# Kernel tuning notes

Hardware: AMD Instinct MI355X
Metric: run time of the kernel (lower is better)

The kernel has to match this reference:

```python
import jax, jax.numpy as jnp
import numpy as np

HIDDEN, MSG, KEY, ROUNDS = 256, 64, 16, 2
LN_EPS = 1e-5


def _orthogonal(key, shape, gain):
    # mimic torch orthogonal_ init (exact values don't matter for correctness testing)
    a = jax.random.normal(key, shape, dtype=jnp.float32)
    q, r = jnp.linalg.qr(a.T if shape[0] < shape[1] else a)
    q = q * jnp.sign(jnp.diag(r))
    if shape[0] < shape[1]:
        q = q.T
    return gain * q[:shape[0], :shape[1]]


def setup_inputs() -> dict:
    key = jax.random.key(0)
    ks = jax.random.split(key, 6)
    g = float(np.sqrt(2.0))
    N = 8192
    return {
        "hidden_states": jax.random.normal(ks[0], (N, HIDDEN), dtype=jnp.float32),
        "W_msg": _orthogonal(ks[1], (MSG, HIDDEN), g),
        "b_msg": jnp.zeros((MSG,), jnp.float32),
        "W_key": _orthogonal(ks[2], (KEY, HIDDEN), g),
        "b_key": jnp.zeros((KEY,), jnp.float32),
        "W_qry": _orthogonal(ks[3], (KEY, HIDDEN), g),
        "b_qry": jnp.zeros((KEY,), jnp.float32),
        "W_agg": _orthogonal(ks[4], (HIDDEN, HIDDEN + MSG), g),
        "b_agg": jnp.zeros((HIDDEN,), jnp.float32),
        "ln_g": jnp.ones((HIDDEN,), jnp.float32),
        "ln_b": jnp.zeros((HIDDEN,), jnp.float32),
    }


def reference(hidden_states, W_msg, b_msg, W_key, b_key, W_qry, b_qry,
              W_agg, b_agg, ln_g, ln_b):
    inv_sqrt_k = 1.0 / np.sqrt(KEY)
    h = hidden_states
    attn = None
    for _ in range(ROUNDS):
        msgs = h @ W_msg.T + b_msg          # (N, MSG)
        keys = h @ W_key.T + b_key          # (N, KEY)
        qrys = h @ W_qry.T + b_qry          # (N, KEY)
        scores = (qrys @ keys.T) * inv_sqrt_k  # (N, N)
        attn = jax.nn.softmax(scores, axis=-1)
        agg_msg = attn @ msgs               # (N, MSG)
        combined = jnp.concatenate([h, agg_msg], axis=-1)  # (N, HIDDEN+MSG)
        z = combined @ W_agg.T + b_agg      # (N, HIDDEN)
        mu = jnp.mean(z, axis=-1, keepdims=True)
        var = jnp.mean(jnp.square(z - mu), axis=-1, keepdims=True)
        h = jax.nn.relu(ln_g * (z - mu) * jax.lax.rsqrt(var + LN_EPS) + ln_b)
    return h, attn
```

## Files before the change

### kernel.cpp

```cpp
#include <hip/hip_runtime.h>

constexpr int H = 256, MSGC = 64;
constexpr float LN_EPS = 1e-5f;
constexpr float QSCALE = 0.25f * 1.4426950408889634f;

typedef __attribute__((ext_vector_type(8))) short bf16x8;
typedef __attribute__((ext_vector_type(4))) float f32x4;

__device__ inline ushort f2bf(float x) {
    union { float f; unsigned u; } v; v.f = x;
    unsigned r = v.u + 0x7fffu + ((v.u >> 16) & 1u);
    return (ushort)(r >> 16);
}
__device__ inline float bf2f(ushort h) {
    union { unsigned u; float f; } v; v.u = ((unsigned)h) << 16;
    return v.f;
}
__device__ inline bf16x8 pack_bf16x8(float4 f0, float4 f1) {
    union { unsigned u[4]; bf16x8 v; } cv;
    asm("v_cvt_pk_bf16_f32 %0, %1, %2" : "=v"(cv.u[0]) : "v"(f0.x), "v"(f0.y));
    asm("v_cvt_pk_bf16_f32 %0, %1, %2" : "=v"(cv.u[1]) : "v"(f0.z), "v"(f0.w));
    asm("v_cvt_pk_bf16_f32 %0, %1, %2" : "=v"(cv.u[2]) : "v"(f1.x), "v"(f1.y));
    asm("v_cvt_pk_bf16_f32 %0, %1, %2" : "=v"(cv.u[3]) : "v"(f1.z), "v"(f1.w));
    return cv.v;
}

__global__ __launch_bounds__(256) void prep_kernel(
    const float* __restrict__ Wm, const float* __restrict__ Wk,
    const float* __restrict__ Wq, const float* __restrict__ Wa,
    ushort* __restrict__ Wph, ushort* __restrict__ Wpl,
    ushort* __restrict__ Wfh, ushort* __restrict__ Wfl)
{
    const int t = threadIdx.x, b = blockIdx.x;
    if (b < 48) {
        const int tile = b >> 3, kc = b & 7;
#pragma unroll
        for (int j2 = 0; j2 < 2; ++j2) {
            const int idx = t * 2 + j2;
            const int l = idx >> 3, e = idx & 7;
            const int col = tile * 16 + (l & 15);
            const int k = kc * 32 + (l >> 4) * 8 + e;
            float v;
            if (col < 64)      v = Wm[(size_t)col * H + k];
            else if (col < 80) v = Wk[(size_t)(col - 64) * H + k];
            else               v = QSCALE * Wq[(size_t)(col - 80) * H + k];
            ushort hi = f2bf(v);
            Wph[(size_t)b * 512 + idx] = hi;
            Wpl[(size_t)b * 512 + idx] = f2bf(v - bf2f(hi));
        }
    } else {
        const int unit = b - 48;
        const int ctg = unit / 10, kc = unit % 10;
#pragma unroll
        for (int j2 = 0; j2 < 2; ++j2) {
            const int idx = t * 2 + j2;
            const int l = idx >> 3, e = idx & 7;
            const int col = ctg * 16 + (l & 15);
            const int k = kc * 32 + (l >> 4) * 8 + e;
            const float v = Wa[(size_t)col * 320 + k];
            ushort hi = f2bf(v);
            Wfh[(size_t)unit * 512 + idx] = hi;
            Wfl[(size_t)unit * 512 + idx] = f2bf(v - bf2f(hi));
        }
    }
}

__global__ __launch_bounds__(128) void proj_kernel(
    const float* __restrict__ h,
    const ushort* __restrict__ Wph, const ushort* __restrict__ Wpl,
    const float* __restrict__ bm, const float* __restrict__ bk, const float* __restrict__ bq,
    ushort* __restrict__ msgsF, ushort* __restrict__ kh, ushort* __restrict__ kl,
    ushort* __restrict__ qh, ushort* __restrict__ ql, int n)
{
    constexpr int AST = 264;
    __shared__ ushort Ahi[16 * AST];
    __shared__ ushort Alo[16 * AST];
    const int t = threadIdx.x, lane = t & 63, w = t >> 6;
    const int gq = lane >> 4, c = lane & 15;
    const int r0 = blockIdx.x * 16;
    const float4* hsrc = (const float4*)(h + (size_t)r0 * H);
#pragma unroll
    for (int u = 0; u < 8; ++u) {
        const int idx = t + 128 * u;
        const int row = idx >> 6, c4 = idx & 63;
        float4 v = hsrc[idx];
        ushort4 hi, lo;
        hi.x = f2bf(v.x); lo.x = f2bf(v.x - bf2f(hi.x));
        hi.y = f2bf(v.y); lo.y = f2bf(v.y - bf2f(hi.y));
        hi.z = f2bf(v.z); lo.z = f2bf(v.z - bf2f(hi.z));
        hi.w = f2bf(v.w); lo.w = f2bf(v.w - bf2f(hi.w));
        *(ushort4*)&Ahi[row * AST + c4 * 4] = hi;
        *(ushort4*)&Alo[row * AST + c4 * 4] = lo;
    }
    __syncthreads();
    f32x4 acc[3] = {{0,0,0,0},{0,0,0,0},{0,0,0,0}};
    for (int kc = 0; kc < 8; ++kc) {
        const bf16x8 afh = *(const bf16x8*)&Ahi[c * AST + kc * 32 + gq * 8];
        const bf16x8 afl = *(const bf16x8*)&Alo[c * AST + kc * 32 + gq * 8];
#pragma unroll
        for (int ct = 0; ct < 3; ++ct) {
            const int unit = (w * 3 + ct) * 8 + kc;
            const bf16x8 whi = *(const bf16x8*)(Wph + (size_t)unit * 512 + lane * 8);
            const bf16x8 wlo = *(const bf16x8*)(Wpl + (size_t)unit * 512 + lane * 8);
            acc[ct] = __builtin_amdgcn_mfma_f32_16x16x32_bf16(afh, whi, acc[ct], 0, 0, 0);
            acc[ct] = __builtin_amdgcn_mfma_f32_16x16x32_bf16(afh, wlo, acc[ct], 0, 0, 0);
            acc[ct] = __builtin_amdgcn_mfma_f32_16x16x32_bf16(afl, whi, acc[ct], 0, 0, 0);
        }
    }
#pragma unroll
    for (int ct = 0; ct < 3; ++ct) {
        const int tile = w * 3 + ct;
        if (tile < 4) {
            const float bb = bm[tile * 16 + c];
#pragma unroll
            for (int r = 0; r < 4; ++r) {
                const int j = r0 + gq * 4 + r;
                const size_t idx = ((size_t)(j >> 5) * 4 + tile) * 512
                                 + ((j >> 3) & 3) * 128 + c * 8 + (j & 7);
                msgsF[idx] = f2bf(acc[ct][r] + bb);
            }
        } else if (tile == 4) {
            const float bb = bk[c];
#pragma unroll
            for (int r = 0; r < 4; ++r) {
                const int j = r0 + gq * 4 + r;
                const float v = acc[ct][r] + bb;
                const ushort hi = f2bf(v);
                kh[(size_t)j * 16 + c] = hi;
                kl[(size_t)j * 16 + c] = f2bf(v - bf2f(hi));
            }
        } else {
            const float bb = QSCALE * bq[c];
#pragma unroll
            for (int r = 0; r < 4; ++r) {
                const int j = r0 + gq * 4 + r;
                const float v = acc[ct][r] + bb;
                const ushort hi = f2bf(v);
                qh[(size_t)j * 16 + c] = hi;
                ql[(size_t)j * 16 + c] = f2bf(v - bf2f(hi));
            }
        }
    }
}

__device__ __forceinline__ void loadK(bf16x8* dst, const ushort* __restrict__ kh,
                                      int j0, int g, int c) {
#pragma unroll
    for (int js = 0; js < 4; ++js)
        dst[js] = *(const bf16x8*)(kh + (size_t)(j0 + js * 16 + c) * 16 + 8 * (g & 1));
}

__device__ __forceinline__ void qk_tile(const bf16x8* b1s, const ushort* __restrict__ kl,
                                        int j0, int g, int c, bf16x8 a1, bf16x8 a2,
                                        const bf16x8 zer, f32x4* pd) {
    const f32x4 z4 = {0.f, 0.f, 0.f, 0.f};
    bf16x8 b2s[4];
#pragma unroll
    for (int js = 0; js < 4; ++js)
        b2s[js] = (g < 2) ? *(const bf16x8*)(kl + (size_t)(j0 + js * 16 + c) * 16 + 8 * g) : zer;
#pragma unroll
    for (int js = 0; js < 4; ++js) {
        pd[js] = __builtin_amdgcn_mfma_f32_16x16x32_bf16(a1, b1s[js], z4, 0, 0, 0);
        pd[js] = __builtin_amdgcn_mfma_f32_16x16x32_bf16(a2, b2s[js], pd[js], 0, 0, 0);
    }
}

__device__ __forceinline__ void pv_tile(const float* __restrict__ P,
                                        const ushort* __restrict__ msgsF,
                                        int j0, int g, int c, int w, int lane, f32x4* accv) {
#pragma unroll
    for (int ks = 0; ks < 2; ++ks) {
        const int arow = w * 16 + c;
        const int sw = (arow & 7) << 2;
        const int colb = ks * 32 + 8 * g;
        float4 f0 = *(const float4*)&P[arow * 64 + ((colb) ^ sw)];
        float4 f1 = *(const float4*)&P[arow * 64 + ((colb + 4) ^ sw)];
        bf16x8 af = pack_bf16x8(f0, f1);
        const size_t mbase = ((size_t)(j0 >> 5) + ks) * 4;
#pragma unroll
        for (int mt = 0; mt < 4; ++mt) {
            bf16x8 bfr = *((const bf16x8*)(msgsF + (mbase + mt) * 512) + lane);
            accv[mt] = __builtin_amdgcn_mfma_f32_16x16x32_bf16(af, bfr, accv[mt], 0, 0, 0);
        }
    }
}

__global__ __launch_bounds__(256) void flash1_kernel(
    const ushort* __restrict__ qh, const ushort* __restrict__ ql,
    const ushort* __restrict__ kh, const ushort* __restrict__ kl,
    const ushort* __restrict__ msgsF,
    float* __restrict__ aggO, float* __restrict__ aggL, int n)
{
    __shared__ float P[64 * 64];
    const int t = threadIdx.x, lane = t & 63, w = t >> 6;
    const int g = lane >> 4, c = lane & 15;
    const int i0 = blockIdx.x * 64;
    bf16x8 zer = {0,0,0,0,0,0,0,0};
    f32x4 z4 = {0.f, 0.f, 0.f, 0.f};
    const ushort* qsrc = (g < 2) ? qh : ql;
    bf16x8 a1 = *(const bf16x8*)(qsrc + (size_t)(i0 + w * 16 + c) * 16 + 8 * (g & 1));
    bf16x8 a2 = (g < 2) ? a1 : zer;
    float l[4] = {0.f, 0.f, 0.f, 0.f};
    f32x4 accv[4] = {z4, z4, z4, z4};
    const int nj = n / 8, jb = blockIdx.y * nj;
    bf16x8 bA[4], bB[4];
    loadK(bA, kh, jb, g, c);
    for (int p = 0; p < 8; ++p) {
        const int t0 = jb + p * 128, t1 = t0 + 64;
        const int t2 = (p < 7) ? t0 + 128 : t1;
        loadK(bB, kh, t1, g, c);
        {
            f32x4 pd[4];
            qk_tile(bA, kl, t0, g, c, a1, a2, zer, pd);
#pragma unroll
            for (int js = 0; js < 4; ++js)
#pragma unroll
                for (int r = 0; r < 4; ++r) {
                    const int row = w * 16 + g * 4 + r;
                    float pp = exp2f(pd[js][r]);
                    l[r] += pp;
                    P[row * 64 + ((js * 16 + c) ^ ((row & 7) << 2))] = pp;
                }
            pv_tile(P, msgsF, t0, g, c, w, lane, accv);
        }
        loadK(bA, kh, t2, g, c);
        {
            f32x4 pd[4];
            qk_tile(bB, kl, t1, g, c, a1, a2, zer, pd);
#pragma unroll
            for (int js = 0; js < 4; ++js)
#pragma unroll
                for (int r = 0; r < 4; ++r) {
                    const int row = w * 16 + g * 4 + r;
                    float pp = exp2f(pd[js][r]);
                    l[r] += pp;
                    P[row * 64 + ((js * 16 + c) ^ ((row & 7) << 2))] = pp;
                }
            pv_tile(P, msgsF, t1, g, c, w, lane, accv);
        }
    }
#pragma unroll
    for (int r = 0; r < 4; ++r)
#pragma unroll
        for (int d2 = 1; d2 < 16; d2 <<= 1) l[r] += __shfl_xor(l[r], d2, 64);
#pragma unroll
    for (int mt = 0; mt < 4; ++mt)
#pragma unroll
        for (int r = 0; r < 4; ++r)
            aggO[((size_t)blockIdx.y * n + i0 + w * 16 + g * 4 + r) * MSGC + mt * 16 + c] = accv[mt][r];
    if (c == 0) {
#pragma unroll
        for (int r = 0; r < 4; ++r)
            aggL[(size_t)blockIdx.y * n + i0 + w * 16 + g * 4 + r] = l[r];
    }
}

__global__ __launch_bounds__(256) void stats_kernel(
    const ushort* __restrict__ qh, const ushort* __restrict__ ql,
    const ushort* __restrict__ kh, const ushort* __restrict__ kl,
    float* __restrict__ rowl_p, int n)
{
    const int t = threadIdx.x, lane = t & 63, w = t >> 6;
    const int g = lane >> 4, c = lane & 15;
    const int iq = blockIdx.x * 64 + w * 16 + c;
    bf16x8 zer = {0,0,0,0,0,0,0,0};
    const ushort* qsrc = (g < 2) ? qh : ql;
    bf16x8 a1 = *(const bf16x8*)(qsrc + (size_t)iq * 16 + 8 * (g & 1));
    bf16x8 a2 = (g < 2) ? a1 : zer;
    const int nj = n / 8, jb = blockIdx.y * nj;
    float l[4] = {0.f, 0.f, 0.f, 0.f};
    bf16x8 bA[4], bB[4];
    loadK(bA, kh, jb, g, c);
    for (int p = 0; p < 8; ++p) {
        const int t0 = jb + p * 128, t1 = t0 + 64;
        const int t2 = (p < 7) ? t0 + 128 : t1;
        loadK(bB, kh, t1, g, c);
        {
            f32x4 pd[4];
            qk_tile(bA, kl, t0, g, c, a1, a2, zer, pd);
#pragma unroll
            for (int js = 0; js < 4; ++js)
#pragma unroll
                for (int r = 0; r < 4; ++r) l[r] += exp2f(pd[js][r]);
        }
        loadK(bA, kh, t2, g, c);
        {
            f32x4 pd[4];
            qk_tile(bB, kl, t1, g, c, a1, a2, zer, pd);
#pragma unroll
            for (int js = 0; js < 4; ++js)
#pragma unroll
                for (int r = 0; r < 4; ++r) l[r] += exp2f(pd[js][r]);
        }
    }
#pragma unroll
    for (int r = 0; r < 4; ++r)
#pragma unroll
        for (int d2 = 1; d2 < 16; d2 <<= 1) l[r] += __shfl_xor(l[r], d2, 64);
    if (c == 0) {
        const int q0 = blockIdx.x * 64 + w * 16 + g * 4;
#pragma unroll
        for (int r = 0; r < 4; ++r)
            rowl_p[(size_t)blockIdx.y * n + q0 + r] = l[r];
    }
}

__global__ __launch_bounds__(256) void pass2_kernel(
    const ushort* __restrict__ qh, const ushort* __restrict__ ql,
    const ushort* __restrict__ kh, const ushort* __restrict__ kl,
    const ushort* __restrict__ msgsF, const float* __restrict__ rowl_p,
    float* __restrict__ aggO, float* __restrict__ attn, int n)
{
    __shared__ float P[64 * 64];
    const int t = threadIdx.x, lane = t & 63, w = t >> 6;
    const int g = lane >> 4, c = lane & 15;
    const int i0 = blockIdx.x * 64;
    bf16x8 zer = {0,0,0,0,0,0,0,0};
    f32x4 z4 = {0.f, 0.f, 0.f, 0.f};
    const ushort* qsrc = (g < 2) ? qh : ql;
    bf16x8 a1 = *(const bf16x8*)(qsrc + (size_t)(i0 + w * 16 + c) * 16 + 8 * (g & 1));
    bf16x8 a2 = (g < 2) ? a1 : zer;
    float rinv_r[4];
#pragma unroll
    for (int r = 0; r < 4; ++r) {
        const int q = i0 + w * 16 + g * 4 + r;
        float L = 0.f;
#pragma unroll
        for (int p = 0; p < 8; ++p) L += rowl_p[(size_t)p * n + q];
        rinv_r[r] = 1.f / L;
    }
    f32x4 accv[4] = {z4, z4, z4, z4};
    const int nj = n / 8, jb = blockIdx.y * nj;
    bf16x8 bA[4], bB[4];
    loadK(bA, kh, jb, g, c);
    for (int p = 0; p < 8; ++p) {
        const int t0 = jb + p * 128, t1 = t0 + 64;
        const int t2 = (p < 7) ? t0 + 128 : t1;
        loadK(bB, kh, t1, g, c);
#pragma unroll
        for (int half = 0; half < 2; ++half) {
            const int j0 = half ? t1 : t0;
            f32x4 pd[4];
            qk_tile(half ? bB : bA, kl, j0, g, c, a1, a2, zer, pd);
            if (half == 0) loadK(bA, kh, t2, g, c);
#pragma unroll
            for (int js = 0; js < 4; ++js)
#pragma unroll
                for (int r = 0; r < 4; ++r) {
                    const int row = w * 16 + g * 4 + r;
                    const float pp = exp2f(pd[js][r]) * rinv_r[r];
                    P[row * 64 + ((js * 16 + c) ^ ((row & 7) << 2))] = pp;
                }
#pragma unroll
            for (int u = 0; u < 16; ++u) {
                const int row = w * 16 + u;
                const int sw = (row & 7) << 2;
                attn[(size_t)(i0 + row) * n + j0 + lane] = P[row * 64 + (lane ^ sw)];
            }
            pv_tile(P, msgsF, j0, g, c, w, lane, accv);
        }
    }
#pragma unroll
    for (int mt = 0; mt < 4; ++mt)
#pragma unroll
        for (int r = 0; r < 4; ++r) {
            const int row = w * 16 + g * 4 + r;
            aggO[((size_t)blockIdx.y * n + i0 + row) * MSGC + mt * 16 + c] = accv[mt][r];
        }
}

template <bool FLASH>
__global__ __launch_bounds__(256) void aggln_kernel(
    const float* __restrict__ h, const float* __restrict__ aggO,
    const float* __restrict__ aggL,
    const ushort* __restrict__ Wfh, const ushort* __restrict__ Wfl,
    const float* __restrict__ ba,
    const float* __restrict__ gg, const float* __restrict__ bb,
    float* __restrict__ hout, int n)
{
    constexpr int AST = 328;
    __shared__ ushort Ahi[16 * AST];
    __shared__ ushort Alo[16 * AST];
    __shared__ float Linv[16];
    __shared__ float red1[16][4], red2[16][4];
    const int t = threadIdx.x, lane = t & 63, w = t >> 6;
    const int gq = lane >> 4, c = lane & 15;
    const int r0 = blockIdx.x * 16;
    const float4* hsrc = (const float4*)(h + (size_t)r0 * H);
#pragma unroll
    for (int u = 0; u < 4; ++u) {
        const int idx = t + 256 * u;
        const int row = idx >> 6, c4 = idx & 63;
        float4 v = hsrc[idx];
        ushort4 hi, lo;
        hi.x = f2bf(v.x); lo.x = f2bf(v.x - bf2f(hi.x));
        hi.y = f2bf(v.y); lo.y = f2bf(v.y - bf2f(hi.y));
        hi.z = f2bf(v.z); lo.z = f2bf(v.z - bf2f(hi.z));
        hi.w = f2bf(v.w); lo.w = f2bf(v.w - bf2f(hi.w));
        *(ushort4*)&Ahi[row * AST + c4 * 4] = hi;
        *(ushort4*)&Alo[row * AST + c4 * 4] = lo;
    }
    if (FLASH && t < 16) {
        float L = 0.f;
#pragma unroll
        for (int p = 0; p < 8; ++p) L += aggL[(size_t)p * n + r0 + t];
        Linv[t] = 1.f / L;
    }
    __syncthreads();
    {
        const int row = t >> 4, c4 = t & 15;
        float4 s = {0.f, 0.f, 0.f, 0.f};
#pragma unroll
        for (int p = 0; p < 8; ++p) {
            const float4 v = *(const float4*)(aggO + (size_t)p * n * MSGC
                               + (size_t)(r0 + row) * MSGC + c4 * 4);
            s.x += v.x; s.y += v.y; s.z += v.z; s.w += v.w;
        }
        if (FLASH) { const float li = Linv[row]; s.x *= li; s.y *= li; s.z *= li; s.w *= li; }
        ushort4 hi, lo;
        hi.x = f2bf(s.x); lo.x = f2bf(s.x - bf2f(hi.x));
        hi.y = f2bf(s.y); lo.y = f2bf(s.y - bf2f(hi.y));
        hi.z = f2bf(s.z); lo.z = f2bf(s.z - bf2f(hi.z));
        hi.w = f2bf(s.w); lo.w = f2bf(s.w - bf2f(hi.w));
        *(ushort4*)&Ahi[row * AST + 256 + c4 * 4] = hi;
        *(ushort4*)&Alo[row * AST + 256 + c4 * 4] = lo;
    }
    __syncthreads();
    f32x4 acc[4] = {{0,0,0,0},{0,0,0,0},{0,0,0,0},{0,0,0,0}};
    for (int kc = 0; kc < 10; ++kc) {
        const bf16x8 afh = *(const bf16x8*)&Ahi[c * AST + kc * 32 + gq * 8];
        const bf16x8 afl = *(const bf16x8*)&Alo[c * AST + kc * 32 + gq * 8];
#pragma unroll
        for (int ct = 0; ct < 4; ++ct) {
            const int ctg = w * 4 + ct;
            const bf16x8 whi = *(const bf16x8*)(Wfh + ((size_t)(ctg * 10 + kc)) * 512 + lane * 8);
            const bf16x8 wlo = *(const bf16x8*)(Wfl + ((size_t)(ctg * 10 + kc)) * 512 + lane * 8);
            acc[ct] = __builtin_amdgcn_mfma_f32_16x16x32_bf16(afh, whi, acc[ct], 0, 0, 0);
            acc[ct] = __builtin_amdgcn_mfma_f32_16x16x32_bf16(afh, wlo, acc[ct], 0, 0, 0);
            acc[ct] = __builtin_amdgcn_mfma_f32_16x16x32_bf16(afl, whi, acc[ct], 0, 0, 0);
        }
    }
    float bav[4], gv[4], bv[4];
#pragma unroll
    for (int ct = 0; ct < 4; ++ct) {
        const int col = w * 64 + ct * 16 + c;
        bav[ct] = ba[col]; gv[ct] = gg[col]; bv[ct] = bb[col];
    }
#pragma unroll
    for (int ct = 0; ct < 4; ++ct) {
        acc[ct][0] += bav[ct]; acc[ct][1] += bav[ct];
        acc[ct][2] += bav[ct]; acc[ct][3] += bav[ct];
    }
#pragma unroll
    for (int r = 0; r < 4; ++r) {
        float s1 = 0.f, s2 = 0.f;
#pragma unroll
        for (int ct = 0; ct < 4; ++ct) { const float v = acc[ct][r]; s1 += v; s2 += v * v; }
#pragma unroll
        for (int d = 1; d < 16; d <<= 1) { s1 += __shfl_xor(s1, d, 64); s2 += __shfl_xor(s2, d, 64); }
        if (c == 0) { red1[gq * 4 + r][w] = s1; red2[gq * 4 + r][w] = s2; }
    }
    __syncthreads();
#pragma unroll
    for (int r = 0; r < 4; ++r) {
        const int row = gq * 4 + r;
        const float s1 = red1[row][0] + red1[row][1] + red1[row][2] + red1[row][3];
        const float s2 = red2[row][0] + red2[row][1] + red2[row][2] + red2[row][3];
        const float mu = s1 * (1.f / 256.f);
        const float var = s2 * (1.f / 256.f) - mu * mu;
        const float rs = rsqrtf(var + LN_EPS);
#pragma unroll
        for (int ct = 0; ct < 4; ++ct) {
            float o = (acc[ct][r] - mu) * rs * gv[ct] + bv[ct];
            hout[(size_t)(r0 + row) * H + w * 64 + ct * 16 + c] = fmaxf(o, 0.f);
        }
    }
}

extern "C" void kernel_launch(void* const* d_in, const int* in_sizes, int n_in,
                              void* d_out, int out_size, void* d_ws, size_t ws_size,
                              hipStream_t stream)
{
    const float* hs = (const float*)d_in[0];
    const float* Wm = (const float*)d_in[1];
    const float* bm = (const float*)d_in[2];
    const float* Wk = (const float*)d_in[3];
    const float* bk = (const float*)d_in[4];
    const float* Wq = (const float*)d_in[5];
    const float* bq = (const float*)d_in[6];
    const float* Wa = (const float*)d_in[7];
    const float* ba = (const float*)d_in[8];
    const float* lg = (const float*)d_in[9];
    const float* lb = (const float*)d_in[10];
    const int n = in_sizes[0] / H;

    char* wp = (char*)d_ws;
    auto alloc = [&](size_t bytes) { void* p = (void*)wp; wp += (bytes + 255) & ~(size_t)255; return p; };
    float*  h2     = (float*)alloc((size_t)n * H * 4);
    ushort* qh     = (ushort*)alloc((size_t)n * 16 * 2);
    ushort* ql     = (ushort*)alloc((size_t)n * 16 * 2);
    ushort* kh     = (ushort*)alloc((size_t)n * 16 * 2);
    ushort* kl     = (ushort*)alloc((size_t)n * 16 * 2);
    ushort* msgsF  = (ushort*)alloc((size_t)MSGC * n * 2);
    float*  rowl_p = (float*)alloc((size_t)8 * n * 4);
    float*  aggO   = (float*)alloc((size_t)8 * n * MSGC * 4);
    float*  aggL   = (float*)alloc((size_t)8 * n * 4);
    ushort* Wph    = (ushort*)alloc((size_t)48 * 512 * 2);
    ushort* Wpl    = (ushort*)alloc((size_t)48 * 512 * 2);
    ushort* Wfh    = (ushort*)alloc((size_t)160 * 512 * 2);
    ushort* Wfl    = (ushort*)alloc((size_t)160 * 512 * 2);

    float* hOut = (float*)d_out;
    float* attn = hOut + (size_t)n * H;

    prep_kernel<<<208, 256, 0, stream>>>(Wm, Wk, Wq, Wa, Wph, Wpl, Wfh, Wfl);

    proj_kernel<<<n / 16, 128, 0, stream>>>(hs, Wph, Wpl, bm, bk, bq, msgsF, kh, kl, qh, ql, n);
    flash1_kernel<<<dim3(n / 64, 8), 256, 0, stream>>>(qh, ql, kh, kl, msgsF,
                                                       aggO, aggL, n);
    aggln_kernel<true><<<n / 16, 256, 0, stream>>>(hs, aggO, aggL, Wfh, Wfl,
                                                   ba, lg, lb, h2, n);
    proj_kernel<<<n / 16, 128, 0, stream>>>(h2, Wph, Wpl, bm, bk, bq, msgsF, kh, kl, qh, ql, n);
    stats_kernel<<<dim3(n / 64, 8), 256, 0, stream>>>(qh, ql, kh, kl, rowl_p, n);
    pass2_kernel<<<dim3(n / 64, 8), 256, 0, stream>>>(qh, ql, kh, kl, msgsF,
                                                      rowl_p, aggO, attn, n);
    aggln_kernel<false><<<n / 16, 256, 0, stream>>>(h2, aggO, aggL, Wfh, Wfl,
                                                    ba, lg, lb, hOut, n);
}
```

Baseline: 271.9 us.

## Double-buffer P tiles to overlap QK exp with PV MFMA; vectorize attn writes

flash1 and pass2 now keep two LDS buffers for the probability tile. The QK^T of the next 64-key tile is issued while the PV product on the previous tile runs, software-pipelining the exp/store stage against the MFMA stage. The attn store in pass2 now uses float4 writes of 4 rows per wave instead of scalar per-row writes. Launch bounds now request 4 blocks per CU; the extra 16KB of LDS per block and the tighter register budget may limit occupancy or cause spills.

```diff
diff --git a/kernel.cpp b/kernel.cpp
--- a/kernel.cpp
+++ b/kernel.cpp
@@ -185,13 +185,52 @@
     }
 }
 
-__global__ __launch_bounds__(256) void flash1_kernel(
+__device__ __forceinline__ void expstore(const f32x4* pd, float* Pbuf, float* l,
+                                         int w, int g, int c) {
+#pragma unroll
+    for (int js = 0; js < 4; ++js)
+#pragma unroll
+        for (int r = 0; r < 4; ++r) {
+            const int row = w * 16 + g * 4 + r;
+            const float pp = exp2f(pd[js][r]);
+            l[r] += pp;
+            Pbuf[row * 64 + ((js * 16 + c) ^ ((row & 7) << 2))] = pp;
+        }
+}
+
+__device__ __forceinline__ void expstore_n(const f32x4* pd, float* Pbuf, const float* rinv,
+                                           int w, int g, int c) {
+#pragma unroll
+    for (int js = 0; js < 4; ++js)
+#pragma unroll
+        for (int r = 0; r < 4; ++r) {
+            const int row = w * 16 + g * 4 + r;
+            const float pp = exp2f(pd[js][r]) * rinv[r];
+            Pbuf[row * 64 + ((js * 16 + c) ^ ((row & 7) << 2))] = pp;
+        }
+}
+
+__device__ __forceinline__ void attn_write(const float* __restrict__ Pbuf,
+                                           float* __restrict__ attn,
+                                           int i0, int j0, int n, int lane, int w) {
+    const int c4 = lane & 15;
+#pragma unroll
+    for (int u = 0; u < 4; ++u) {
+        const int row = w * 16 + u * 4 + (lane >> 4);
+        const int sw = (row & 7) << 2;
+        float4 v = *(const float4*)&Pbuf[row * 64 + ((c4 * 4) ^ sw)];
+        *(float4*)(attn + (size_t)(i0 + row) * n + j0 + c4 * 4) = v;
+    }
+}
+
+__global__ __launch_bounds__(256, 4) void flash1_kernel(
     const ushort* __restrict__ qh, const ushort* __restrict__ ql,
     const ushort* __restrict__ kh, const ushort* __restrict__ kl,
     const ushort* __restrict__ msgsF,
     float* __restrict__ aggO, float* __restrict__ aggL, int n)
 {
-    __shared__ float P[64 * 64];
+    __shared__ float P0[64 * 64];
+    __shared__ float P1[64 * 64];
     const int t = threadIdx.x, lane = t & 63, w = t >> 6;
     const int g = lane >> 4, c = lane & 15;
     const int i0 = blockIdx.x * 64;
@@ -205,40 +244,37 @@
     const int nj = n / 8, jb = blockIdx.y * nj;
     bf16x8 bA[4], bB[4];
     loadK(bA, kh, jb, g, c);
-    for (int p = 0; p < 8; ++p) {
-        const int t0 = jb + p * 128, t1 = t0 + 64;
-        const int t2 = (p < 7) ? t0 + 128 : t1;
-        loadK(bB, kh, t1, g, c);
+    loadK(bB, kh, jb + 64, g, c);
+    {
+        f32x4 pd[4];
+        qk_tile(bA, kl, jb, g, c, a1, a2, zer, pd);
+        expstore(pd, P0, l, w, g, c);
+    }
+    loadK(bA, kh, jb + 128, g, c);
+    {
+        f32x4 pd[4];
+        qk_tile(bB, kl, jb + 64, g, c, a1, a2, zer, pd);
+        pv_tile(P0, msgsF, jb, g, c, w, lane, accv);
+        expstore(pd, P1, l, w, g, c);
+    }
+    for (int p = 1; p < 8; ++p) {
+        const int tA = jb + p * 128, tB = tA + 64;
+        loadK(bB, kh, tB, g, c);
         {
             f32x4 pd[4];
-            qk_tile(bA, kl, t0, g, c, a1, a2, zer, pd);
-#pragma unroll
-            for (int js = 0; js < 4; ++js)
-#pragma unroll
-                for (int r = 0; r < 4; ++r) {
-                    const int row = w * 16 + g * 4 + r;
-                    float pp = exp2f(pd[js][r]);
-                    l[r] += pp;
-                    P[row * 64 + ((js * 16 + c) ^ ((row & 7) << 2))] = pp;
-                }
-            pv_tile(P, msgsF, t0, g, c, w, lane, accv);
-        }
-        loadK(bA, kh, t2, g, c);
+            qk_tile(bA, kl, tA, g, c, a1, a2, zer, pd);
+            pv_tile(P1, msgsF, tA - 64, g, c, w, lane, accv);
+            expstore(pd, P0, l, w, g, c);
+        }
+        loadK(bA, kh, (p < 7) ? tA + 128 : tB, g, c);
         {
             f32x4 pd[4];
-            qk_tile(bB, kl, t1, g, c, a1, a2, zer, pd);
-#pragma unroll
-            for (int js = 0; js < 4; ++js)
-#pragma unroll
-                for (int r = 0; r < 4; ++r) {
-                    const int row = w * 16 + g * 4 + r;
-                    float pp = exp2f(pd[js][r]);
-                    l[r] += pp;
-                    P[row * 64 + ((js * 16 + c) ^ ((row & 7) << 2))] = pp;
-                }
-            pv_tile(P, msgsF, t1, g, c, w, lane, accv);
-        }
-    }
+            qk_tile(bB, kl, tB, g, c, a1, a2, zer, pd);
+            pv_tile(P0, msgsF, tA, g, c, w, lane, accv);
+            expstore(pd, P1, l, w, g, c);
+        }
+    }
+    pv_tile(P1, msgsF, jb + nj - 64, g, c, w, lane, accv);
 #pragma unroll
     for (int r = 0; r < 4; ++r)
 #pragma unroll
@@ -255,7 +291,7 @@
     }
 }
 
-__global__ __launch_bounds__(256) void stats_kernel(
+__global__ __launch_bounds__(256, 4) void stats_kernel(
     const ushort* __restrict__ qh, const ushort* __restrict__ ql,
     const ushort* __restrict__ kh, const ushort* __restrict__ kl,
     float* __restrict__ rowl_p, int n)
@@ -305,13 +341,14 @@
     }
 }
 
-__global__ __launch_bounds__(256) void pass2_kernel(
+__global__ __launch_bounds__(256, 4) void pass2_kernel(
     const ushort* __restrict__ qh, const ushort* __restrict__ ql,
     const ushort* __restrict__ kh, const ushort* __restrict__ kl,
     const ushort* __restrict__ msgsF, const float* __restrict__ rowl_p,
     float* __restrict__ aggO, float* __restrict__ attn, int n)
 {
-    __shared__ float P[64 * 64];
+    __shared__ float P0[64 * 64];
+    __shared__ float P1[64 * 64];
     const int t = threadIdx.x, lane = t & 63, w = t >> 6;
     const int g = lane >> 4, c = lane & 15;
     const int i0 = blockIdx.x * 64;
@@ -320,46 +357,54 @@
     const ushort* qsrc = (g < 2) ? qh : ql;
     bf16x8 a1 = *(const bf16x8*)(qsrc + (size_t)(i0 + w * 16 + c) * 16 + 8 * (g & 1));
     bf16x8 a2 = (g < 2) ? a1 : zer;
-    float rinv_r[4];
+    float rinv[4];
 #pragma unroll
     for (int r = 0; r < 4; ++r) {
         const int q = i0 + w * 16 + g * 4 + r;
         float L = 0.f;
 #pragma unroll
         for (int p = 0; p < 8; ++p) L += rowl_p[(size_t)p * n + q];
-        rinv_r[r] = 1.f / L;
+        rinv[r] = 1.f / L;
     }
     f32x4 accv[4] = {z4, z4, z4, z4};
     const int nj = n / 8, jb = blockIdx.y * nj;
     bf16x8 bA[4], bB[4];
     loadK(bA, kh, jb, g, c);
-    for (int p = 0; p < 8; ++p) {
-        const int t0 = jb + p * 128, t1 = t0 + 64;
-        const int t2 = (p < 7) ? t0 + 128 : t1;
-        loadK(bB, kh, t1, g, c);
-#pragma unroll
-        for (int half = 0; half < 2; ++half) {
-            const int j0 = half ? t1 : t0;
+    loadK(bB, kh, jb + 64, g, c);
+    {
+        f32x4 pd[4];
+        qk_tile(bA, kl, jb, g, c, a1, a2, zer, pd);
+        expstore_n(pd, P0, rinv, w, g, c);
+    }
+    loadK(bA, kh, jb + 128, g, c);
+    {
+        f32x4 pd[4];
+        qk_tile(bB, kl, jb + 64, g, c, a1, a2, zer, pd);
+        attn_write(P0, attn, i0, jb, n, lane, w);
+        pv_tile(P0, msgsF, jb, g, c, w, lane, accv);
+        expstore_n(pd, P1, rinv, w, g, c);
+    }
+    for (int p = 1; p < 8; ++p) {
+        const int tA = jb + p * 128, tB = tA + 64;
+        loadK(bB, kh, tB, g, c);
+        {
             f32x4 pd[4];
-            qk_tile(half ? bB : bA, kl, j0, g, c, a1, a2, zer, pd);
-            if (half == 0) loadK(bA, kh, t2, g, c);
-#pragma unroll
-            for (int js = 0; js < 4; ++js)
-#pragma unroll
-                for (int r = 0; r < 4; ++r) {
-                    const int row = w * 16 + g * 4 + r;
-                    const float pp = exp2f(pd[js][r]) * rinv_r[r];
-                    P[row * 64 + ((js * 16 + c) ^ ((row & 7) << 2))] = pp;
-                }
-#pragma unroll
-            for (int u = 0; u < 16; ++u) {
-                const int row = w * 16 + u;
-                const int sw = (row & 7) << 2;
-                attn[(size_t)(i0 + row) * n + j0 + lane] = P[row * 64 + (lane ^ sw)];
-            }
-            pv_tile(P, msgsF, j0, g, c, w, lane, accv);
-        }
-    }
+            qk_tile(bA, kl, tA, g, c, a1, a2, zer, pd);
+            attn_write(P1, attn, i0, tA - 64, n, lane, w);
+            pv_tile(P1, msgsF, tA - 64, g, c, w, lane, accv);
+            expstore_n(pd, P0, rinv, w, g, c);
+        }
+        loadK(bA, kh, (p < 7) ? tA + 128 : tB, g, c);
+        {
+            f32x4 pd[4];
+            qk_tile(bB, kl, tB, g, c, a1, a2, zer, pd);
+            attn_write(P0, attn, i0, tA, n, lane, w);
+            pv_tile(P0, msgsF, tA, g, c, w, lane, accv);
+            expstore_n(pd, P1, rinv, w, g, c);
+        }
+    }
+    attn_write(P1, attn, i0, jb + nj - 64, n, lane, w);
+    pv_tile(P1, msgsF, jb + nj - 64, g, c, w, lane, accv);
 #pragma unroll
     for (int mt = 0; mt < 4; ++mt)
 #pragma unroll
```

After: 244.5 us. 1.11x faster.
